# Optimization experiments

Measured on AMD Instinct MI355X. Metric: run time of the kernel, lower is better.

Reference implementation:

```python
import jax, jax.numpy as jnp
import numpy as np

C = 64  # in_dim

def _dwpw(x, w_dw, w_pw):
    # depthwise 1x1x1 conv (groups=C, no bias) == per-channel scale
    x = x * w_dw[None, :, None, None, None]
    # pointwise 1x1x1 conv (no bias) == channel mixing matmul
    return jnp.einsum('bcdhw,oc->bodhw', x, w_pw)

def setup_inputs() -> dict:
    key = jax.random.key(0)
    ks = jax.random.split(key, 8)
    B, D, H, W = 2, 16, 16, 16
    x = jax.random.normal(ks[0], (B, C, D, H, W), dtype=jnp.float32)
    s = 1.0 / np.sqrt(C)
    q_dw = jax.random.normal(ks[1], (C,), dtype=jnp.float32) * s
    q_pw = jax.random.normal(ks[2], (C, C), dtype=jnp.float32) * s
    k_dw = jax.random.normal(ks[3], (C,), dtype=jnp.float32) * s
    k_pw = jax.random.normal(ks[4], (C, C), dtype=jnp.float32) * s
    v_dw = jax.random.normal(ks[5], (C,), dtype=jnp.float32) * s
    v_pw = jax.random.normal(ks[6], (C, C), dtype=jnp.float32) * s
    gamma = jnp.zeros((1,), dtype=jnp.float32) + 0.1  # nonzero so output depends on attention
    return {"x": x, "q_dw": q_dw, "q_pw": q_pw, "k_dw": k_dw, "k_pw": k_pw,
            "v_dw": v_dw, "v_pw": v_pw, "gamma": gamma}

def reference(x, q_dw, q_pw, k_dw, k_pw, v_dw, v_pw, gamma):
    B, Cc, D, H, W = x.shape
    N = D * H * W
    q = _dwpw(x, q_dw, q_pw).reshape(B, Cc, N)  # [B,C,N]
    k = _dwpw(x, k_dw, k_pw).reshape(B, Cc, N)
    v = _dwpw(x, v_dw, v_pw).reshape(B, Cc, N)
    # energy[b,i,j] = sum_c q[b,c,i] * k[b,c,j]
    energy = jnp.einsum('bci,bcj->bij', q, k)
    attn = jax.nn.softmax(energy, axis=-1)  # softmax over j
    # out[b,c,i] = sum_j v[b,c,j] * attn[b,i,j]
    out = jnp.einsum('bcj,bij->bci', v, attn).reshape(B, Cc, D, H, W)
    return gamma * out + x
```

## Files before the change

### kernel.cpp

```cpp
#include <hip/hip_runtime.h>
#include <hip/hip_bf16.h>

#define NPOS 4096
#define CDIM 64
#define BATCH 2
#define JSPLIT 16
#define JCHUNK (NPOS / JSPLIT)
#define RPB 128
#define PSTR 72

typedef __attribute__((ext_vector_type(8))) short bf16x8;
typedef __attribute__((ext_vector_type(4))) float f32x4;
typedef __attribute__((ext_vector_type(4))) unsigned int u32x4;
typedef __attribute__((ext_vector_type(2))) unsigned int u32x2;

static __device__ __forceinline__ unsigned int fbits(float f) {
    union { float f; unsigned int u; } v; v.f = f; return v.u;
}
static __device__ __forceinline__ float bffloat(unsigned int hi16) {
    union { unsigned int u; float f; } v; v.u = hi16; return v.f;
}
static __device__ __forceinline__ unsigned int pk2bf(float a, float b) {
    return ((fbits(a) + 0x8000u) >> 16) | ((fbits(b) + 0x8000u) & 0xffff0000u);
}
static __device__ __forceinline__ short f2bs(float f) {
    return (short)(unsigned short)((fbits(f) + 0x8000u) >> 16);
}

__global__ __launch_bounds__(256) void weff_kernel(
    const float* __restrict__ q_dw, const float* __restrict__ q_pw,
    const float* __restrict__ k_dw, const float* __restrict__ k_pw,
    const float* __restrict__ v_dw, const float* __restrict__ v_pw,
    short* __restrict__ Wg)
{
    int i = blockIdx.x * 256 + threadIdx.x;
    if (i >= 192 * 64) return;
    int op = i >> 6, c = i & 63, p = op >> 6, o = op & 63;
    const float* pw = (p == 0) ? q_pw : (p == 1) ? k_pw : v_pw;
    const float* dw = (p == 0) ? q_dw : (p == 1) ? k_dw : v_dw;
    Wg[i] = f2bs(pw[o * 64 + c] * dw[c]);
}

__global__ __launch_bounds__(64) void qkv_kernel(
    const float* __restrict__ x, const short* __restrict__ Wg,
    short* __restrict__ qT, short* __restrict__ kT, short* __restrict__ vM)
{
    const int bid  = blockIdx.x;
    const int p    = bid >> 9;
    const int np   = bid & 511;
    const int b    = np >> 8;
    const int n0   = (np & 255) << 4;
    const int lane = threadIdx.x;
    const int col  = lane & 15;
    const int quad = lane >> 4;
    const int n    = n0 + col;

    bf16x8 xf0, xf1;
    #pragma unroll
    for (int j = 0; j < 8; ++j) {
        xf0[j] = f2bs(x[(size_t)(b * CDIM + quad * 8 + j) * NPOS + n]);
        xf1[j] = f2bs(x[(size_t)(b * CDIM + 32 + quad * 8 + j) * NPOS + n]);
    }

    if (p < 2) {
        short* dst = p ? kT : qT;
        #pragma unroll
        for (int os = 0; os < 4; ++os) {
            const short* wp = Wg + (p * 64 + os * 16 + col) * 64 + quad * 8;
            bf16x8 wf0 = *(const bf16x8*)wp;
            bf16x8 wf1 = *(const bf16x8*)(wp + 32);
            f32x4 d = (f32x4){0.f, 0.f, 0.f, 0.f};
            d = __builtin_amdgcn_mfma_f32_16x16x32_bf16(wf0, xf0, d, 0, 0, 0);
            d = __builtin_amdgcn_mfma_f32_16x16x32_bf16(wf1, xf1, d, 0, 0, 0);
            *(u32x2*)(dst + (size_t)(b * NPOS + n) * CDIM + os * 16 + quad * 4) =
                (u32x2){pk2bf(d[0], d[1]), pk2bf(d[2], d[3])};
        }
    } else {
        #pragma unroll
        for (int os = 0; os < 4; ++os) {
            const short* wp = Wg + (128 + os * 16 + col) * 64 + quad * 8;
            bf16x8 wf0 = *(const bf16x8*)wp;
            bf16x8 wf1 = *(const bf16x8*)(wp + 32);
            f32x4 d = (f32x4){0.f, 0.f, 0.f, 0.f};
            d = __builtin_amdgcn_mfma_f32_16x16x32_bf16(xf0, wf0, d, 0, 0, 0);
            d = __builtin_amdgcn_mfma_f32_16x16x32_bf16(xf1, wf1, d, 0, 0, 0);
            *(u32x2*)(vM + (size_t)(b * CDIM + os * 16 + col) * NPOS + n0 + quad * 4) =
                (u32x2){pk2bf(d[0], d[1]), pk2bf(d[2], d[3])};
        }
    }
}

__global__ __launch_bounds__(256) void attn_kernel(
    const short* __restrict__ qT, const short* __restrict__ kT,
    const short* __restrict__ vM,
    unsigned short* __restrict__ Opart, float* __restrict__ lacc)
{
    const int gid  = blockIdx.x;
    const int jc   = gid & (JSPLIT - 1);
    const int rb   = (gid >> 4) & 31;
    const int b    = gid >> 9;
    const int t    = threadIdx.x;
    const int wave = t >> 6;
    const int lane = t & 63;
    const int col  = lane & 15;
    const int quad = lane >> 4;

    __shared__ __align__(16) short Pw[4][32 * PSTR];

    const short* qTb = qT + (size_t)b * NPOS * CDIM;
    const short* kTb = kT + (size_t)b * NPOS * CDIM;
    const short* vb  = vM + (size_t)b * CDIM * NPOS;

    const int i0 = rb * RPB + wave * 32;

    bf16x8 qf[2][2];
    #pragma unroll
    for (int rs = 0; rs < 2; ++rs) {
        const short* qp = qTb + (size_t)(i0 + rs * 16 + col) * CDIM + quad * 8;
        qf[rs][0] = *(const bf16x8*)qp;
        qf[rs][1] = *(const bf16x8*)(qp + 32);
    }

    f32x4 oacc[2][4];
    #pragma unroll
    for (int rs = 0; rs < 2; ++rs)
        #pragma unroll
        for (int cb = 0; cb < 4; ++cb) oacc[rs][cb] = (f32x4){0.f, 0.f, 0.f, 0.f};
    float lp[2] = {0.f, 0.f};

    short* Pme = Pw[wave];

    for (int jt = 0; jt < JCHUNK / 64; ++jt) {
        const int j0 = jc * JCHUNK + jt * 64;

        #pragma unroll
        for (int ct = 0; ct < 4; ++ct) {
            const short* kp = kTb + (size_t)(j0 + ct * 16 + col) * CDIM + quad * 8;
            bf16x8 kf0 = *(const bf16x8*)kp;
            bf16x8 kf1 = *(const bf16x8*)(kp + 32);
            #pragma unroll
            for (int rs = 0; rs < 2; ++rs) {
                f32x4 a = (f32x4){0.f, 0.f, 0.f, 0.f};
                a = __builtin_amdgcn_mfma_f32_16x16x32_bf16(kf0, qf[rs][0], a, 0, 0, 0);
                a = __builtin_amdgcn_mfma_f32_16x16x32_bf16(kf1, qf[rs][1], a, 0, 0, 0);
                float p0 = __expf(a[0]), p1 = __expf(a[1]);
                float p2 = __expf(a[2]), p3 = __expf(a[3]);
                lp[rs] += (p0 + p1) + (p2 + p3);
                *(u32x2*)(Pme + (rs * 16 + col) * PSTR + ct * 16 + quad * 4) =
                    (u32x2){pk2bf(p0, p1), pk2bf(p2, p3)};
            }
        }
        asm volatile("" ::: "memory");

        bf16x8 pf[2][2];
        #pragma unroll
        for (int rs = 0; rs < 2; ++rs) {
            const short* pp = Pme + (rs * 16 + col) * PSTR + quad * 8;
            pf[rs][0] = *(const bf16x8*)pp;
            pf[rs][1] = *(const bf16x8*)(pp + 32);
        }
        asm volatile("" ::: "memory");

        #pragma unroll
        for (int cb = 0; cb < 4; ++cb) {
            const short* vp = vb + (size_t)(cb * 16 + col) * NPOS + j0 + quad * 8;
            bf16x8 vf0 = *(const bf16x8*)vp;
            bf16x8 vf1 = *(const bf16x8*)(vp + 32);
            #pragma unroll
            for (int rs = 0; rs < 2; ++rs) {
                oacc[rs][cb] = __builtin_amdgcn_mfma_f32_16x16x32_bf16(vf0, pf[rs][0], oacc[rs][cb], 0, 0, 0);
                oacc[rs][cb] = __builtin_amdgcn_mfma_f32_16x16x32_bf16(vf1, pf[rs][1], oacc[rs][cb], 0, 0, 0);
            }
        }
    }

    #pragma unroll
    for (int rs = 0; rs < 2; ++rs) {
        lp[rs] += __shfl_xor(lp[rs], 16, 64);
        lp[rs] += __shfl_xor(lp[rs], 32, 64);
    }
    if (quad == 0) {
        #pragma unroll
        for (int rs = 0; rs < 2; ++rs)
            lacc[(size_t)(jc * BATCH + b) * NPOS + i0 + rs * 16 + col] = lp[rs];
    }

    unsigned short* Ob = Opart + (size_t)(jc * BATCH + b) * CDIM * NPOS;
    #pragma unroll
    for (int rs = 0; rs < 2; ++rs)
        #pragma unroll
        for (int cb = 0; cb < 4; ++cb)
            #pragma unroll
            for (int r = 0; r < 4; ++r)
                Ob[(size_t)(cb * 16 + quad * 4 + r) * NPOS + i0 + rs * 16 + col] =
                    (unsigned short)f2bs(oacc[rs][cb][r]);
}

__global__ __launch_bounds__(256) void combine_kernel(
    const unsigned short* __restrict__ Opart, const float* __restrict__ lacc,
    const float* __restrict__ x, const float* __restrict__ gamma,
    float* __restrict__ out)
{
    int b  = blockIdx.x >> 7;
    int n0 = (blockIdx.x & 127) << 5;
    __shared__ float linv[32];
    int t = threadIdx.x;
    if (t < 32) {
        float s = 0.f;
        #pragma unroll
        for (int jc = 0; jc < JSPLIT; ++jc)
            s += lacc[(size_t)(jc * BATCH + b) * NPOS + n0 + t];
        linv[t] = gamma[0] / s;
    }
    __syncthreads();

    int c = t >> 2, ns = (t & 3) * 8;
    float acc[8];
    #pragma unroll
    for (int k = 0; k < 8; ++k) acc[k] = 0.f;
    #pragma unroll
    for (int jc = 0; jc < JSPLIT; ++jc) {
        const unsigned short* Ob = Opart + ((size_t)(jc * BATCH + b) * CDIM + c) * NPOS + n0 + ns;
        u32x4 w = *(const u32x4*)Ob;
        #pragma unroll
        for (int j = 0; j < 4; ++j) {
            acc[2 * j]     += bffloat(w[j] << 16);
            acc[2 * j + 1] += bffloat(w[j] & 0xffff0000u);
        }
    }
    const float* xb = x + ((size_t)b * CDIM + c) * NPOS + n0 + ns;
    float* ob = out + ((size_t)b * CDIM + c) * NPOS + n0 + ns;
    #pragma unroll
    for (int k = 0; k < 2; ++k) {
        f32x4 x4 = *(const f32x4*)(xb + k * 4);
        f32x4 r;
        #pragma unroll
        for (int j = 0; j < 4; ++j)
            r[j] = fmaf(acc[k * 4 + j], linv[ns + k * 4 + j], x4[j]);
        *(f32x4*)(ob + k * 4) = r;
    }
}

extern "C" void kernel_launch(void* const* d_in, const int* in_sizes, int n_in,
                              void* d_out, int out_size, void* d_ws, size_t ws_size,
                              hipStream_t stream) {
    const float* x     = (const float*)d_in[0];
    const float* q_dw  = (const float*)d_in[1];
    const float* q_pw  = (const float*)d_in[2];
    const float* k_dw  = (const float*)d_in[3];
    const float* k_pw  = (const float*)d_in[4];
    const float* v_dw  = (const float*)d_in[5];
    const float* v_pw  = (const float*)d_in[6];
    const float* gamma = (const float*)d_in[7];
    float* out = (float*)d_out;

    char* ws = (char*)d_ws;
    short* qT             = (short*)(ws);
    short* kT             = (short*)(ws + (1u << 20));
    short* vM             = (short*)(ws + (2u << 20));
    short* Wg             = (short*)(ws + (3u << 20));
    unsigned short* Opart = (unsigned short*)(ws + (3u << 20) + (1u << 16));
    float* lacc           = (float*)(ws + (3u << 20) + (1u << 16) +
                                     (size_t)JSPLIT * BATCH * CDIM * NPOS * 2);

    weff_kernel<<<48, 256, 0, stream>>>(q_dw, q_pw, k_dw, k_pw, v_dw, v_pw, Wg);
    qkv_kernel<<<3 * BATCH * 256, 64, 0, stream>>>(x, Wg, qT, kT, vM);
    attn_kernel<<<BATCH * 32 * JSPLIT, 256, 0, stream>>>(qT, kT, vM, Opart, lacc);
    combine_kernel<<<BATCH * 128, 256, 0, stream>>>(Opart, lacc, x, gamma, out);
}
```

Measured before the change: 119.9 us.

## Fuse weight prep into QKV kernel and double attention key split

Removes the separate weight-folding kernel launch by computing the depthwise-scaled pointwise weights inline in the QKV projection kernel. Doubles JSPLIT so the attention kernel launches twice as many blocks, each covering a smaller key chunk, and adds an occupancy hint to its launch bounds. The aim is to cut one launch and fill more of the GPU during attention, at the cost of redundant weight arithmetic per block and twice as much partial output for the combine kernel to read.

After: 128.8 us. +7.4%, slower.

```diff
diff --git a/kernel.cpp b/kernel.cpp
--- a/kernel.cpp
+++ b/kernel.cpp
@@ -4,7 +4,7 @@
 #define NPOS 4096
 #define CDIM 64
 #define BATCH 2
-#define JSPLIT 16
+#define JSPLIT 32
 #define JCHUNK (NPOS / JSPLIT)
 #define RPB 128
 #define PSTR 72
@@ -27,22 +27,11 @@
     return (short)(unsigned short)((fbits(f) + 0x8000u) >> 16);
 }
 
-__global__ __launch_bounds__(256) void weff_kernel(
+__global__ __launch_bounds__(64) void qkv_kernel(
+    const float* __restrict__ x,
     const float* __restrict__ q_dw, const float* __restrict__ q_pw,
     const float* __restrict__ k_dw, const float* __restrict__ k_pw,
     const float* __restrict__ v_dw, const float* __restrict__ v_pw,
-    short* __restrict__ Wg)
-{
-    int i = blockIdx.x * 256 + threadIdx.x;
-    if (i >= 192 * 64) return;
-    int op = i >> 6, c = i & 63, p = op >> 6, o = op & 63;
-    const float* pw = (p == 0) ? q_pw : (p == 1) ? k_pw : v_pw;
-    const float* dw = (p == 0) ? q_dw : (p == 1) ? k_dw : v_dw;
-    Wg[i] = f2bs(pw[o * 64 + c] * dw[c]);
-}
-
-__global__ __launch_bounds__(64) void qkv_kernel(
-    const float* __restrict__ x, const short* __restrict__ Wg,
     short* __restrict__ qT, short* __restrict__ kT, short* __restrict__ vM)
 {
     const int bid  = blockIdx.x;
@@ -55,33 +44,36 @@
     const int quad = lane >> 4;
     const int n    = n0 + col;
 
+    const float* pw = (p == 0) ? q_pw : (p == 1) ? k_pw : v_pw;
+    const float* dw = (p == 0) ? q_dw : (p == 1) ? k_dw : v_dw;
+
     bf16x8 xf0, xf1;
+    float dv0[8], dv1[8];
     #pragma unroll
     for (int j = 0; j < 8; ++j) {
         xf0[j] = f2bs(x[(size_t)(b * CDIM + quad * 8 + j) * NPOS + n]);
         xf1[j] = f2bs(x[(size_t)(b * CDIM + 32 + quad * 8 + j) * NPOS + n]);
-    }
-
-    if (p < 2) {
-        short* dst = p ? kT : qT;
-        #pragma unroll
-        for (int os = 0; os < 4; ++os) {
-            const short* wp = Wg + (p * 64 + os * 16 + col) * 64 + quad * 8;
-            bf16x8 wf0 = *(const bf16x8*)wp;
-            bf16x8 wf1 = *(const bf16x8*)(wp + 32);
-            f32x4 d = (f32x4){0.f, 0.f, 0.f, 0.f};
+        dv0[j] = dw[quad * 8 + j];
+        dv1[j] = dw[32 + quad * 8 + j];
+    }
+
+    #pragma unroll
+    for (int os = 0; os < 4; ++os) {
+        const float* pr = pw + (os * 16 + col) * 64 + quad * 8;
+        bf16x8 wf0, wf1;
+        #pragma unroll
+        for (int j = 0; j < 8; ++j) {
+            wf0[j] = f2bs(pr[j] * dv0[j]);
+            wf1[j] = f2bs(pr[32 + j] * dv1[j]);
+        }
+        f32x4 d = (f32x4){0.f, 0.f, 0.f, 0.f};
+        if (p < 2) {
             d = __builtin_amdgcn_mfma_f32_16x16x32_bf16(wf0, xf0, d, 0, 0, 0);
             d = __builtin_amdgcn_mfma_f32_16x16x32_bf16(wf1, xf1, d, 0, 0, 0);
+            short* dst = p ? kT : qT;
             *(u32x2*)(dst + (size_t)(b * NPOS + n) * CDIM + os * 16 + quad * 4) =
                 (u32x2){pk2bf(d[0], d[1]), pk2bf(d[2], d[3])};
-        }
-    } else {
-        #pragma unroll
-        for (int os = 0; os < 4; ++os) {
-            const short* wp = Wg + (128 + os * 16 + col) * 64 + quad * 8;
-            bf16x8 wf0 = *(const bf16x8*)wp;
-            bf16x8 wf1 = *(const bf16x8*)(wp + 32);
-            f32x4 d = (f32x4){0.f, 0.f, 0.f, 0.f};
+        } else {
             d = __builtin_amdgcn_mfma_f32_16x16x32_bf16(xf0, wf0, d, 0, 0, 0);
             d = __builtin_amdgcn_mfma_f32_16x16x32_bf16(xf1, wf1, d, 0, 0, 0);
             *(u32x2*)(vM + (size_t)(b * CDIM + os * 16 + col) * NPOS + n0 + quad * 4) =
@@ -90,15 +82,15 @@
     }
 }
 
-__global__ __launch_bounds__(256) void attn_kernel(
+__global__ __launch_bounds__(256, 4) void attn_kernel(
     const short* __restrict__ qT, const short* __restrict__ kT,
     const short* __restrict__ vM,
     unsigned short* __restrict__ Opart, float* __restrict__ lacc)
 {
     const int gid  = blockIdx.x;
     const int jc   = gid & (JSPLIT - 1);
-    const int rb   = (gid >> 4) & 31;
-    const int b    = gid >> 9;
+    const int rb   = (gid >> 5) & 31;
+    const int b    = gid >> 10;
     const int t    = threadIdx.x;
     const int wave = t >> 6;
     const int lane = t & 63;
@@ -258,13 +250,12 @@
     short* qT             = (short*)(ws);
     short* kT             = (short*)(ws + (1u << 20));
     short* vM             = (short*)(ws + (2u << 20));
-    short* Wg             = (short*)(ws + (3u << 20));
-    unsigned short* Opart = (unsigned short*)(ws + (3u << 20) + (1u << 16));
-    float* lacc           = (float*)(ws + (3u << 20) + (1u << 16) +
+    unsigned short* Opart = (unsigned short*)(ws + (3u << 20));
+    float* lacc           = (float*)(ws + (3u << 20) +
                                      (size_t)JSPLIT * BATCH * CDIM * NPOS * 2);
 
-    weff_kernel<<<48, 256, 0, stream>>>(q_dw, q_pw, k_dw, k_pw, v_dw, v_pw, Wg);
-    qkv_kernel<<<3 * BATCH * 256, 64, 0, stream>>>(x, Wg, qT, kT, vM);
+    qkv_kernel<<<3 * BATCH * 256, 64, 0, stream>>>(
+        x, q_dw, q_pw, k_dw, k_pw, v_dw, v_pw, qT, kT, vM);
     attn_kernel<<<BATCH * 32 * JSPLIT, 256, 0, stream>>>(qT, kT, vM, Opart, lacc);
     combine_kernel<<<BATCH * 128, 256, 0, stream>>>(Opart, lacc, x, gamma, out);
 }
```
